# Performance work log

Hardware: AMD Instinct MI355X
Metric: run time of the kernel (lower is better)

The kernel has to match this reference:

```python
import jax, jax.numpy as jnp
import numpy as np

B, C, D, H, W = 4096, 128, 9, 8, 8  # batch, in_dims, d_emb, fmap_size, fmap_size
EPS = 1e-10


def setup_inputs() -> dict:
    key = jax.random.key(0)
    k1, k2 = jax.random.split(key)
    fcn_activations = jax.random.normal(k1, (B, C, H, W), dtype=jnp.float32)
    # precomputed spatial kernel buffer (emb2 in the torch module): [1, out_dims, H, W]
    emb2 = jax.random.normal(k2, (1, C * D, H, W), dtype=jnp.float32)
    return {"fcn_activations": fcn_activations, "emb2": emb2}


def reference(fcn_activations, emb2):
    b, c, h, w = fcn_activations.shape
    d = emb2.shape[1] // c  # d_emb
    # idx1 = arange(c*d)//d, i.e. channel i is repeated d times consecutively.
    # gather + elementwise mult + spatial sum == contraction below (no big emb1 intermediate):
    kern = emb2.reshape(c, d, h, w)
    out = jnp.einsum('bchw,cdhw->bcd', fcn_activations, kern).reshape(b, c * d)
    # L2Norm over last dim
    norm = jnp.sqrt(jnp.sum(out * out, axis=-1) + EPS)
    return out / norm[:, None]
```

## Files before the change

### kernel.cpp

```cpp
#include <hip/hip_runtime.h>


constexpr int B_TOT = 4096;
constexpr int C_CH  = 128;
constexpr int D_EMB = 9;
constexpr int THREADS = 256;
constexpr int GPB = 32;
constexpr int NCH = 4;
constexpr int RB  = 2;
constexpr int ROWF = C_CH * D_EMB;

__device__ __forceinline__ float reduce8_hw(float p) {
    p += __int_as_float(__builtin_amdgcn_mov_dpp(__float_as_int(p), 0xB1,  0xf, 0xf, true));
    p += __int_as_float(__builtin_amdgcn_mov_dpp(__float_as_int(p), 0x4E,  0xf, 0xf, true));
    p += __int_as_float(__builtin_amdgcn_mov_dpp(__float_as_int(p), 0x141, 0xf, 0xf, true));
    return p;
}

__global__ __launch_bounds__(THREADS, 2)
void esenc_fused(const float* __restrict__ fcn,
                 const float* __restrict__ kern,
                 float* __restrict__ out) {
    __shared__ __align__(16) float tile[RB * ROWF];
    __shared__ float red[4 * RB];
    __shared__ float invn[RB];

    const int tid = threadIdx.x;
    const int l   = tid & 7;
    const int g   = tid >> 3;
    const int w   = tid >> 6;
    const unsigned b0 = blockIdx.x * RB;

    const float4* kern4 = (const float4*)kern;
    const float4* f4    = (const float4*)fcn;

    float s = 0.0f;

#pragma unroll
    for (int ch = 0; ch < NCH; ++ch) {
        const unsigned c = (unsigned)(ch * GPB + g);

        float4 f0[RB], f1[RB];
#pragma unroll
        for (int r = 0; r < RB; ++r) {
            const unsigned fb = ((b0 + (unsigned)r) * C_CH + c) * 16u;
            f0[r] = f4[fb + l];
            f1[r] = f4[fb + 8u + l];
        }

        float keep[D_EMB] = {};
#pragma unroll
        for (int d = 0; d < D_EMB; ++d) {
            const unsigned kb = (c * D_EMB + (unsigned)d) * 16u;
            const float4 k0 = kern4[kb + l];
            const float4 k1 = kern4[kb + 8u + l];
#pragma unroll
            for (int r = 0; r < RB; ++r) {
                float t;
                t = f0[r].x * k0.x;
                t = fmaf(f0[r].y, k0.y, t);
                t = fmaf(f0[r].z, k0.z, t);
                t = fmaf(f0[r].w, k0.w, t);
                t = fmaf(f1[r].x, k1.x, t);
                t = fmaf(f1[r].y, k1.y, t);
                t = fmaf(f1[r].z, k1.z, t);
                t = fmaf(f1[r].w, k1.w, t);
                t = reduce8_hw(t);
                if (l == r) keep[d] = t;
            }
        }

        if (l < RB) {
            const int c_i = ch * GPB + g;
#pragma unroll
            for (int d = 0; d < D_EMB; ++d) {
                tile[l * ROWF + c_i * D_EMB + d] = keep[d];
                s = fmaf(keep[d], keep[d], s);
            }
        }
    }

    s += __shfl_xor(s, 8,  64);
    s += __shfl_xor(s, 16, 64);
    s += __shfl_xor(s, 32, 64);
    if ((tid & 63) < RB) red[w * RB + l] = s;
    __syncthreads();
    if (tid < RB)
        invn[tid] = 1.0f / sqrtf(red[tid] + red[RB + tid] + red[2 * RB + tid]
                                 + red[3 * RB + tid] + 1e-10f);
    __syncthreads();

    const float4* t4 = (const float4*)tile;
    float4* o4 = (float4*)(out + (size_t)b0 * ROWF);
#pragma unroll
    for (int j = 0; j < (RB * ROWF / 4 + THREADS - 1) / THREADS; ++j) {
        const int i = tid + j * THREADS;
        if (i < RB * ROWF / 4) {
            const float inv = invn[i / (ROWF / 4)];
            float4 v = t4[i];
            v.x *= inv; v.y *= inv; v.z *= inv; v.w *= inv;
            o4[i] = v;
        }
    }
}

extern "C" void kernel_launch(void* const* d_in, const int* in_sizes, int n_in,
                              void* d_out, int out_size, void* d_ws, size_t ws_size,
                              hipStream_t stream) {
    const float* fcn  = (const float*)d_in[0];
    const float* kern = (const float*)d_in[1];
    float* out = (float*)d_out;

    dim3 grid(B_TOT / RB), block(THREADS);
    hipLaunchKernelGGL(esenc_fused, grid, block, 0, stream, fcn, kern, out);
}
```

Before: 36.18 us.

## Double RB rows per block and prefetch next channel chunk's activations

Each block now handles four batch rows instead of two, halving the grid and reusing every kernel-weight load across twice as many rows. The activation loads for the next channel chunk are issued before the current chunk's FMAs, so global-load latency overlaps with compute. The cost is higher register pressure from the doubled row count plus the prefetch buffers, which may reduce occupancy under launch_bounds(256,2), and a larger LDS tile.

```diff
diff --git a/kernel.cpp b/kernel.cpp
--- a/kernel.cpp
+++ b/kernel.cpp
@@ -7,7 +7,7 @@
 constexpr int THREADS = 256;
 constexpr int GPB = 32;
 constexpr int NCH = 4;
-constexpr int RB  = 2;
+constexpr int RB  = 4;
 constexpr int ROWF = C_CH * D_EMB;
 
 __device__ __forceinline__ float reduce8_hw(float p) {
@@ -36,16 +36,27 @@
 
     float s = 0.0f;
 
+    float4 p0[RB], p1[RB];
+#pragma unroll
+    for (int r = 0; r < RB; ++r) {
+        const unsigned fb = ((b0 + (unsigned)r) * C_CH + (unsigned)g) * 16u;
+        p0[r] = f4[fb + l];
+        p1[r] = f4[fb + 8u + l];
+    }
+
 #pragma unroll
     for (int ch = 0; ch < NCH; ++ch) {
         const unsigned c = (unsigned)(ch * GPB + g);
 
-        float4 f0[RB], f1[RB];
+        float4 n0[RB], n1[RB];
+        if (ch + 1 < NCH) {
+            const unsigned cn = c + (unsigned)GPB;
 #pragma unroll
-        for (int r = 0; r < RB; ++r) {
-            const unsigned fb = ((b0 + (unsigned)r) * C_CH + c) * 16u;
-            f0[r] = f4[fb + l];
-            f1[r] = f4[fb + 8u + l];
+            for (int r = 0; r < RB; ++r) {
+                const unsigned fb = ((b0 + (unsigned)r) * C_CH + cn) * 16u;
+                n0[r] = f4[fb + l];
+                n1[r] = f4[fb + 8u + l];
+            }
         }
 
         float keep[D_EMB] = {};
@@ -57,26 +68,30 @@
 #pragma unroll
             for (int r = 0; r < RB; ++r) {
                 float t;
-                t = f0[r].x * k0.x;
-                t = fmaf(f0[r].y, k0.y, t);
-                t = fmaf(f0[r].z, k0.z, t);
-                t = fmaf(f0[r].w, k0.w, t);
-                t = fmaf(f1[r].x, k1.x, t);
-                t = fmaf(f1[r].y, k1.y, t);
-                t = fmaf(f1[r].z, k1.z, t);
-                t = fmaf(f1[r].w, k1.w, t);
+                t = p0[r].x * k0.x;
+                t = fmaf(p0[r].y, k0.y, t);
+                t = fmaf(p0[r].z, k0.z, t);
+                t = fmaf(p0[r].w, k0.w, t);
+                t = fmaf(p1[r].x, k1.x, t);
+                t = fmaf(p1[r].y, k1.y, t);
+                t = fmaf(p1[r].z, k1.z, t);
+                t = fmaf(p1[r].w, k1.w, t);
                 t = reduce8_hw(t);
                 if (l == r) keep[d] = t;
             }
         }
 
         if (l < RB) {
-            const int c_i = ch * GPB + g;
 #pragma unroll
             for (int d = 0; d < D_EMB; ++d) {
-                tile[l * ROWF + c_i * D_EMB + d] = keep[d];
+                tile[l * ROWF + (int)c * D_EMB + d] = keep[d];
                 s = fmaf(keep[d], keep[d], s);
             }
+        }
+
+        if (ch + 1 < NCH) {
+#pragma unroll
+            for (int r = 0; r < RB; ++r) { p0[r] = n0[r]; p1[r] = n1[r]; }
         }
     }
 
```

New measurement: 31.99 us. 1.13x faster.

## Process eight batch rows per block with 512 threads and nontemporal I/O

Applied to the files above, without the earlier changes.

Each block now handles eight batch rows (one per lane of the 8-lane group) with 512 threads, so every kernel weight load is reused across eight rows instead of two. All eight lanes now keep and write a result, which removes the idle lanes in the store phase. The shared tile rows are padded by one float4 to avoid bank conflicts. Activation loads and output stores use nontemporal hints to avoid polluting cache. In exchange, register pressure rises and the grid has fewer, larger blocks.

```diff
diff --git a/kernel.cpp b/kernel.cpp
--- a/kernel.cpp
+++ b/kernel.cpp
@@ -1,14 +1,17 @@
 #include <hip/hip_runtime.h>
 
+
+using vf4 = __attribute__((ext_vector_type(4))) float;
 
 constexpr int B_TOT = 4096;
 constexpr int C_CH  = 128;
 constexpr int D_EMB = 9;
-constexpr int THREADS = 256;
-constexpr int GPB = 32;
-constexpr int NCH = 4;
-constexpr int RB  = 2;
-constexpr int ROWF = C_CH * D_EMB;
+constexpr int THREADS = 512;
+constexpr int GPB = 64;
+constexpr int NCH = 2;
+constexpr int RB  = 8;
+constexpr int ROW4 = C_CH * D_EMB / 4;
+constexpr int RSTR4 = ROW4 + 1;
 
 __device__ __forceinline__ float reduce8_hw(float p) {
     p += __int_as_float(__builtin_amdgcn_mov_dpp(__float_as_int(p), 0xB1,  0xf, 0xf, true));
@@ -21,8 +24,8 @@
 void esenc_fused(const float* __restrict__ fcn,
                  const float* __restrict__ kern,
                  float* __restrict__ out) {
-    __shared__ __align__(16) float tile[RB * ROWF];
-    __shared__ float red[4 * RB];
+    __shared__ __align__(16) float tile[RB * RSTR4 * 4];
+    __shared__ float red[8 * RB];
     __shared__ float invn[RB];
 
     const int tid = threadIdx.x;
@@ -31,8 +34,8 @@
     const int w   = tid >> 6;
     const unsigned b0 = blockIdx.x * RB;
 
-    const float4* kern4 = (const float4*)kern;
-    const float4* f4    = (const float4*)fcn;
+    const vf4* kern4 = (const vf4*)kern;
+    const vf4* f4    = (const vf4*)fcn;
 
     float s = 0.0f;
 
@@ -40,20 +43,20 @@
     for (int ch = 0; ch < NCH; ++ch) {
         const unsigned c = (unsigned)(ch * GPB + g);
 
-        float4 f0[RB], f1[RB];
+        vf4 f0[RB], f1[RB];
 #pragma unroll
         for (int r = 0; r < RB; ++r) {
             const unsigned fb = ((b0 + (unsigned)r) * C_CH + c) * 16u;
-            f0[r] = f4[fb + l];
-            f1[r] = f4[fb + 8u + l];
+            f0[r] = __builtin_nontemporal_load(f4 + fb + l);
+            f1[r] = __builtin_nontemporal_load(f4 + fb + 8u + l);
         }
 
-        float keep[D_EMB] = {};
+        float keep[D_EMB];
 #pragma unroll
         for (int d = 0; d < D_EMB; ++d) {
             const unsigned kb = (c * D_EMB + (unsigned)d) * 16u;
-            const float4 k0 = kern4[kb + l];
-            const float4 k1 = kern4[kb + 8u + l];
+            const vf4 k0 = kern4[kb + l];
+            const vf4 k1 = kern4[kb + 8u + l];
 #pragma unroll
             for (int r = 0; r < RB; ++r) {
                 float t;
@@ -70,13 +73,10 @@
             }
         }
 
-        if (l < RB) {
-            const int c_i = ch * GPB + g;
 #pragma unroll
-            for (int d = 0; d < D_EMB; ++d) {
-                tile[l * ROWF + c_i * D_EMB + d] = keep[d];
-                s = fmaf(keep[d], keep[d], s);
-            }
+        for (int d = 0; d < D_EMB; ++d) {
+            tile[l * (RSTR4 * 4) + (int)c * D_EMB + d] = keep[d];
+            s = fmaf(keep[d], keep[d], s);
         }
     }
 
@@ -85,21 +85,26 @@
     s += __shfl_xor(s, 32, 64);
     if ((tid & 63) < RB) red[w * RB + l] = s;
     __syncthreads();
-    if (tid < RB)
-        invn[tid] = 1.0f / sqrtf(red[tid] + red[RB + tid] + red[2 * RB + tid]
-                                 + red[3 * RB + tid] + 1e-10f);
+    if (tid < RB) {
+        float t = 0.0f;
+#pragma unroll
+        for (int j = 0; j < 8; ++j) t += red[j * RB + tid];
+        invn[tid] = 1.0f / sqrtf(t + 1e-10f);
+    }
     __syncthreads();
 
-    const float4* t4 = (const float4*)tile;
-    float4* o4 = (float4*)(out + (size_t)b0 * ROWF);
+    const vf4* t4 = (const vf4*)tile;
+    vf4* o4 = (vf4*)out;
 #pragma unroll
-    for (int j = 0; j < (RB * ROWF / 4 + THREADS - 1) / THREADS; ++j) {
+    for (int j = 0; j < (RB * ROW4 + THREADS - 1) / THREADS; ++j) {
         const int i = tid + j * THREADS;
-        if (i < RB * ROWF / 4) {
-            const float inv = invn[i / (ROWF / 4)];
-            float4 v = t4[i];
+        if (i < RB * ROW4) {
+            const int row = i / ROW4;
+            const int off = i - row * ROW4;
+            const float inv = invn[row];
+            vf4 v = t4[row * RSTR4 + off];
             v.x *= inv; v.y *= inv; v.z *= inv; v.w *= inv;
-            o4[i] = v;
+            __builtin_nontemporal_store(v, o4 + (size_t)(b0 + row) * ROW4 + off);
         }
     }
 }
```

Result: slower. 37.91 us (+4.8%).
